# Performance work log

Hardware: AMD Instinct MI355X
Metric: run time of the kernel (lower is better)

## Reference

```python
import jax, jax.numpy as jnp
import numpy as np
from jax import lax

B, V, C, D, H, W = 1, 5, 32, 48, 128, 160
RATIO = 8


def setup_inputs() -> dict:
    key = jax.random.key(0)
    k1, k2, k3 = jax.random.split(key, 3)
    features = jax.random.normal(k1, (V, B, C, H, W), jnp.float32)
    # proj_matrices[b, v, 0] = 4x4 extrinsic, proj_matrices[b, v, 1, :3, :3] = intrinsic K
    f = 200.0
    K = np.array([[f, 0.0, W / 2.0], [0.0, f, H / 2.0], [0.0, 0.0, 1.0]], np.float32)
    proj = np.zeros((B, V, 2, 4, 4), np.float32)
    for v in range(V):
        E = np.eye(4, dtype=np.float32)
        E[0, 3] = 2.0 * v  # horizontal baseline per source view
        proj[:, v, 0] = E
        P1 = np.eye(4, dtype=np.float32)
        P1[:3, :3] = K
        proj[:, v, 1] = P1
    proj_matrices = jnp.asarray(proj)
    depth_values = jnp.broadcast_to(jnp.linspace(425.0, 935.0, D, dtype=jnp.float32), (B, D))
    mask = jax.random.normal(k2, (B, 9 * RATIO * RATIO, H, W), jnp.float32)
    W_reg = jax.random.normal(k3, (1, C, 3, 3, 3), jnp.float32) * 0.05
    return {"features": features, "proj_matrices": proj_matrices,
            "depth_values": depth_values, "mask": mask, "W_reg": W_reg}


def _combine(p):
    # p: [B,2,4,4] -> K @ E[:3,:4] written into top 3 rows of extrinsic (as in source)
    top = jnp.einsum('bij,bjk->bik', p[:, 1, :3, :3], p[:, 0, :3, :4])
    return p[:, 0].at[:, :3, :4].set(top)


def _bilinear_sample(src, x, y):
    # src [B,C,H,W]; x,y [B,P] pixel coords; zeros padding, align_corners=True
    Bs, Cs, Hs, Ws = src.shape
    x0 = jnp.floor(x)
    y0 = jnp.floor(y)
    wx = x - x0
    wy = y - y0
    src_flat = src.reshape(Bs, Cs, Hs * Ws)

    def gather(xi, yi, w):
        valid = (xi >= 0) & (xi <= Ws - 1) & (yi >= 0) & (yi <= Hs - 1)
        xi_c = jnp.clip(xi, 0, Ws - 1).astype(jnp.int32)
        yi_c = jnp.clip(yi, 0, Hs - 1).astype(jnp.int32)
        idx = (yi_c * Ws + xi_c)[:, None, :]
        vals = jnp.take_along_axis(src_flat, jnp.broadcast_to(idx, (Bs, Cs, idx.shape[-1])), axis=2)
        return vals * (w * valid)[:, None, :]

    return (gather(x0, y0, (1 - wx) * (1 - wy)) + gather(x0 + 1, y0, wx * (1 - wy))
            + gather(x0, y0 + 1, (1 - wx) * wy) + gather(x0 + 1, y0 + 1, wx * wy))


def _homo_warp(src_fea, src_proj, ref_proj, depth_values):
    # faithful homo_warping2: project ref pixel grid at each depth hypothesis into src view
    Bs, Cs, Hs, Ws = src_fea.shape
    Dd = depth_values.shape[1]
    proj = jnp.einsum('bij,bjk->bik', src_proj, jnp.linalg.inv(ref_proj))
    rot = proj[:, :3, :3]
    trans = proj[:, :3, 3]
    ys, xs = jnp.meshgrid(jnp.arange(Hs, dtype=src_fea.dtype), jnp.arange(Ws, dtype=src_fea.dtype), indexing='ij')
    xyz = jnp.stack([xs.ravel(), ys.ravel(), jnp.ones(Hs * Ws, dtype=src_fea.dtype)])  # [3,HW]
    rot_xyz = jnp.einsum('bij,jp->bip', rot, xyz)  # [B,3,HW]
    pts = rot_xyz[:, :, None, :] * depth_values[:, None, :, None] + trans[:, :, None, None]  # [B,3,D,HW]
    gx = pts[:, 0] / pts[:, 2]
    gy = pts[:, 1] / pts[:, 2]
    warped = _bilinear_sample(src_fea, gx.reshape(Bs, -1), gy.reshape(Bs, -1))
    return warped.reshape(Bs, Cs, Dd, Hs, Ws)


def _convex_upsample(depth, mask, r):
    # depth [N,1,H,W], mask [N,9*r*r,H,W] -> [N, r*H, r*W]
    N, _, Hh, Ww = depth.shape
    m = jax.nn.softmax(mask.reshape(N, 1, 9, r, r, Hh, Ww), axis=2)
    dp = jnp.pad(depth, ((0, 0), (0, 0), (1, 1), (1, 1)))
    nb = jnp.stack([dp[:, :, dy:dy + Hh, dx:dx + Ww] for dy in range(3) for dx in range(3)], axis=2)
    up = jnp.sum(m * nb[:, :, :, None, None], axis=2)  # [N,1,r,r,H,W]
    up = up.transpose(0, 1, 4, 2, 5, 3)  # [N,1,H,r,W,r]
    return up.reshape(N, r * Hh, r * Ww)


def reference(features, proj_matrices, depth_values, mask, W_reg):
    num_views = features.shape[0]
    Dd = depth_values.shape[1]
    ref_proj = _combine(proj_matrices[:, 0])
    # variance cost-volume accumulation over views (ref volume broadcast along D)
    vsum = features[0][:, :, None, :, :]
    vsq = vsum ** 2
    for v in range(1, num_views):
        src_proj = _combine(proj_matrices[:, v])
        wv = _homo_warp(features[v], src_proj, ref_proj, depth_values)
        vsum = vsum + wv
        vsq = vsq + wv * wv
    variance = vsq / num_views - (vsum / num_views) ** 2  # [B,C,D,H,W]
    # cost regularization stand-in: 3x3x3 conv C->1, SAME padding
    pre = lax.conv_general_dilated(variance, W_reg, (1, 1, 1), 'SAME',
                                   dimension_numbers=('NCDHW', 'OIDHW', 'NCDHW'))[:, 0]
    prob = jax.nn.softmax(pre, axis=1)  # [B,D,H,W]
    depth = jnp.sum(prob * depth_values[:, :, None, None], axis=1)  # [B,H,W]
    # photometric confidence (no-grad path): sliding sum of 4 along D, pad (1,2)
    pd = jnp.pad(prob, ((0, 0), (1, 2), (0, 0), (0, 0)))
    sum4 = pd[:, 0:Dd] + pd[:, 1:Dd + 1] + pd[:, 2:Dd + 2] + pd[:, 3:Dd + 3]
    di = jnp.sum(prob * jnp.arange(Dd, dtype=prob.dtype)[None, :, None, None], axis=1).astype(jnp.int32)
    di = jnp.clip(di, 0, Dd - 1)
    conf = jax.lax.stop_gradient(jnp.take_along_axis(sum4, di[:, None], axis=1)[:, 0])
    depth_up = _convex_upsample(depth[:, None], mask, RATIO)
    return (depth_up, depth, conf)
```

## Files before the change

kernel.cpp:

```cpp
#include <hip/hip_runtime.h>
#include <hip/hip_bf16.h>


#define NV 5
#define NC 32
#define ND 48
#define NH 128
#define NW 160
#define HW (NH * NW)
#define DHW (ND * HW)

typedef __attribute__((ext_vector_type(2))) float f32x2;
typedef __attribute__((ext_vector_type(4))) float f32x4;
typedef __attribute__((ext_vector_type(2), aligned(4))) float f32x2u;
typedef __attribute__((ext_vector_type(8))) unsigned short u16x8;

#define OFF_M      0
#define OFF_WF     256
#define OFF_DEPTHF 4096
#define OFF_PRE    86016
#define OFF_WV     4018176

__device__ __forceinline__ float bf2f(unsigned short u) {
  uint32_t b = ((uint32_t)u) << 16;
  float f;
  __builtin_memcpy(&f, &b, 4);
  return f;
}

__global__ void k_setup(const float* __restrict__ proj,
                        const float* __restrict__ wreg,
                        float* __restrict__ M, float* __restrict__ wf) {
  if (threadIdx.x != 0) return;
  double P[NV][2][4][4];
  for (int v = 0; v < NV; ++v)
    for (int m = 0; m < 2; ++m)
      for (int i = 0; i < 4; ++i)
        for (int j = 0; j < 4; ++j)
          P[v][m][i][j] = (double)proj[((v * 2 + m) * 4 + i) * 4 + j];
  double C[NV][4][4];
  for (int v = 0; v < NV; ++v) {
    for (int i = 0; i < 4; ++i)
      for (int j = 0; j < 4; ++j) C[v][i][j] = P[v][0][i][j];
    for (int i = 0; i < 3; ++i)
      for (int j = 0; j < 4; ++j) {
        double s = 0.0;
        for (int k = 0; k < 3; ++k) s += P[v][1][i][k] * P[v][0][k][j];
        C[v][i][j] = s;
      }
  }
  double a[4][8];
  for (int i = 0; i < 4; ++i)
    for (int j = 0; j < 4; ++j) { a[i][j] = C[0][i][j]; a[i][j + 4] = (i == j) ? 1.0 : 0.0; }
  for (int col = 0; col < 4; ++col) {
    int piv = col; double best = fabs(a[col][col]);
    for (int r = col + 1; r < 4; ++r) { double v = fabs(a[r][col]); if (v > best) { best = v; piv = r; } }
    if (piv != col)
      for (int j = 0; j < 8; ++j) { double t = a[col][j]; a[col][j] = a[piv][j]; a[piv][j] = t; }
    double pv = a[col][col];
    for (int j = 0; j < 8; ++j) a[col][j] /= pv;
    for (int r = 0; r < 4; ++r) if (r != col) {
      double f = a[r][col];
      for (int j = 0; j < 8; ++j) a[r][j] -= f * a[col][j];
    }
  }
  double inv[4][4];
  for (int i = 0; i < 4; ++i)
    for (int j = 0; j < 4; ++j) inv[i][j] = a[i][j + 4];
  for (int v = 1; v < NV; ++v) {
    float* m = M + (v - 1) * 12;
    for (int i = 0; i < 3; ++i) {
      double r[4] = {0, 0, 0, 0};
      for (int k = 0; k < 4; ++k) {
        double cv = C[v][i][k];
        for (int j = 0; j < 4; ++j) r[j] += cv * inv[k][j];
      }
      m[i * 3 + 0] = (float)r[0]; m[i * 3 + 1] = (float)r[1]; m[i * 3 + 2] = (float)r[2];
      m[9 + i] = (float)r[3];
    }
  }
  for (int c = 0; c < NC; ++c) {
    for (int t = 0; t < 27; ++t) wf[c * 28 + t] = wreg[c * 27 + t];
    wf[c * 28 + 27] = 0.f;
  }
}

__global__ __launch_bounds__(256) void k_warpvar(
    const float* __restrict__ feat,
    const float* __restrict__ depthv,
    const float* __restrict__ M,
    const float* __restrict__ wf,
    __hip_bfloat16* __restrict__ WV)
{
  int idx = blockIdx.x * 256 + threadIdx.x;
  int x = idx % NW;
  int t1 = idx / NW;
  int y = t1 % NH;
  int d = t1 / NH;
  int pix = y * NW + x;
  float xf = (float)x, yf = (float)y;
  float df = depthv[d];

  int   off[4];
  float wA[4], wB[4];
  bool any4 = false;

#pragma unroll
  for (int v = 0; v < 4; ++v) {
    const float* m = M + v * 12;
    float rx = m[0] * xf + m[1] * yf + m[2];
    float ry = m[3] * xf + m[4] * yf + m[5];
    float rz = m[6] * xf + m[7] * yf + m[8];
    float px = rx * df + m[9];
    float py = ry * df + m[10];
    float pz = rz * df + m[11];
    float gx = px / pz;
    float gy = py / pz;
    float y0 = floorf(gy);
    float wy = gy - y0;
    bool two = (wy == 0.f) || (wy == 1.f);
    any4 = any4 || !two;
    float rowf = (wy == 0.f) ? y0 : (y0 + 1.f);
    float x0 = floorf(gx);
    float wx = gx - x0;
    bool yok  = (rowf >= 0.f) && (rowf <= (float)(NH - 1));
    bool x0ok = (x0 >= 0.f) && (x0 <= (float)(NW - 1)) && yok;
    bool x1ok = (x0 >= -1.f) && (x0 <= (float)(NW - 2)) && yok;
    float rc = fminf(fmaxf(rowf, 0.f), (float)(NH - 1));
    float xc = fminf(fmaxf(x0, 0.f), (float)(NW - 1));
    int xi = (int)xc;
    int o = (int)rc * NW + xi;
    bool ddv = (o == HW - 1);
    bool sv  = (x0 >= 0.f) && (xi <= NW - 2);
    o -= ddv ? 1 : 0;
    float w0 = (1.f - wx) * (x0ok ? 1.f : 0.f);
    float w1 = wx * (x1ok ? 1.f : 0.f);
    float wsum = w0 + w1;
    wA[v] = ddv ? 0.f : (sv ? w0 : wsum);
    wB[v] = ddv ? wsum : (sv ? w1 : 0.f);
    off[v] = o;
  }

  f32x2 wv[14];
#pragma unroll
  for (int u = 0; u < 14; ++u) { wv[u].x = 0.f; wv[u].y = 0.f; }

  if (__builtin_expect(any4, 0)) {
    int cidx[16]; float cw[16];
#pragma unroll
    for (int v = 0; v < 4; ++v) {
      const float* m = M + v * 12;
      float rx = m[0] * xf + m[1] * yf + m[2];
      float ry = m[3] * xf + m[4] * yf + m[5];
      float rz = m[6] * xf + m[7] * yf + m[8];
      float px = rx * df + m[9];
      float py = ry * df + m[10];
      float pz = rz * df + m[11];
      float gx = px / pz;
      float gy = py / pz;
      float x0 = floorf(gx), y0 = floorf(gy);
      float wx = gx - x0, wy = gy - y0;
      float cxs[2] = {x0, x0 + 1.f}, cys[2] = {y0, y0 + 1.f};
      float wxs[2] = {1.f - wx, wx}, wys[2] = {1.f - wy, wy};
#pragma unroll
      for (int cy = 0; cy < 2; ++cy)
#pragma unroll
        for (int cx = 0; cx < 2; ++cx) {
          float fx = cxs[cx], fy = cys[cy];
          bool valid = (fx >= 0.f) && (fx <= (float)(NW - 1)) &&
                       (fy >= 0.f) && (fy <= (float)(NH - 1));
          float fxc = fminf(fmaxf(fx, 0.f), (float)(NW - 1));
          float fyc = fminf(fmaxf(fy, 0.f), (float)(NH - 1));
          int xi2 = (int)fxc, yi2 = (int)fyc;
          cidx[v * 4 + cy * 2 + cx] = yi2 * NW + xi2;
          cw[v * 4 + cy * 2 + cx] = wxs[cx] * wys[cy] * (valid ? 1.f : 0.f);
        }
    }
    for (int c = 0; c < NC; ++c) {
      float f0 = feat[c * HW + pix];
      float vs = f0, vq = f0 * f0;
#pragma unroll
      for (int v = 0; v < 4; ++v) {
        const float* fv = feat + ((v + 1) * NC + c) * HW;
        float val = cw[v * 4 + 0] * fv[cidx[v * 4 + 0]]
                  + cw[v * 4 + 1] * fv[cidx[v * 4 + 1]]
                  + cw[v * 4 + 2] * fv[cidx[v * 4 + 2]]
                  + cw[v * 4 + 3] * fv[cidx[v * 4 + 3]];
        vs += val;
        vq += val * val;
      }
      float var = vq * 0.2f - (vs * 0.2f) * (vs * 0.2f);
      const f32x2* wrow = (const f32x2*)(wf + c * 28);
      f32x2 vv; vv.x = var; vv.y = var;
#pragma unroll
      for (int u = 0; u < 14; ++u) wv[u] += wrow[u] * vv;
    }
  } else {
#pragma unroll
    for (int g = 0; g < NC; g += 8) {
      float f0[8];
      f32x2 e[8][4];
#pragma unroll
      for (int cc = 0; cc < 8; ++cc) {
        int c = g + cc;
        f0[cc] = feat[c * HW + pix];
#pragma unroll
        for (int v = 0; v < 4; ++v) {
          const float* fv = feat + ((v + 1) * NC + c) * HW;
          f32x2u t = *(const f32x2u*)(fv + off[v]);
          e[cc][v].x = t.x; e[cc][v].y = t.y;
        }
      }
#pragma unroll
      for (int cc = 0; cc < 8; ++cc) {
        int c = g + cc;
        float vs = f0[cc], vq = f0[cc] * f0[cc];
#pragma unroll
        for (int v = 0; v < 4; ++v) {
          float val = wA[v] * e[cc][v].x + wB[v] * e[cc][v].y;
          vs += val;
          vq += val * val;
        }
        float var = vq * 0.2f - (vs * 0.2f) * (vs * 0.2f);
        const f32x2* wrow = (const f32x2*)(wf + c * 28);
        f32x2 vv; vv.x = var; vv.y = var;
#pragma unroll
        for (int u = 0; u < 14; ++u) wv[u] += wrow[u] * vv;
      }
    }
  }

#pragma unroll
  for (int u = 0; u < 14; ++u) {
    int t0 = 2 * u;
    WV[t0 * DHW + idx] = __float2bfloat16(wv[u].x);
    if (t0 + 1 < 27) WV[(t0 + 1) * DHW + idx] = __float2bfloat16(wv[u].y);
  }
}

__global__ __launch_bounds__(256) void k_conv(const __hip_bfloat16* __restrict__ WV,
                                              float* __restrict__ pre) {
  int t8 = blockIdx.x * 256 + threadIdx.x;
  int x8 = (t8 % (NW / 8)) * 8;
  int r = t8 / (NW / 8);
  int y = r % NH;
  int d = r / NH;

  bool lo_ok = (x8 > 0);
  bool hi_ok = (x8 < NW - 8);
  int xlo = lo_ok ? x8 - 2 : 0;
  int xhi = hi_ok ? x8 + 8 : NW - 8;

  float acc[8];
#pragma unroll
  for (int k = 0; k < 8; ++k) acc[k] = 0.f;

#pragma unroll
  for (int dd = 0; dd < 3; ++dd) {
    int dp = d + dd - 1;
    bool dok = (dp >= 0) && (dp < ND);
    int dpc = min(max(dp, 0), ND - 1);
#pragma unroll
    for (int i = 0; i < 3; ++i) {
      int yp = y + i - 1;
      bool yok = (yp >= 0) && (yp < NH);
      int ypc = min(max(yp, 0), NH - 1);
      float gok = (dok && yok) ? 1.f : 0.f;
      const __hip_bfloat16* base =
          WV + (size_t)(dd * 9 + i * 3) * DHW + (size_t)dpc * HW + ypc * NW;

      u16x8 m0 = *(const u16x8*)(base + x8);
      uint32_t l0; __builtin_memcpy(&l0, base + xlo, 4);
      u16x8 m1 = *(const u16x8*)(base + DHW + x8);
      u16x8 m2 = *(const u16x8*)(base + 2 * (size_t)DHW + x8);
      uint32_t h2; __builtin_memcpy(&h2, base + 2 * (size_t)DHW + xhi, 4);

      float em1 = lo_ok ? bf2f((unsigned short)(l0 >> 16)) : 0.f;
      float e8  = hi_ok ? bf2f((unsigned short)(h2 & 0xffff)) : 0.f;

      acc[0] += gok * (em1 + bf2f(m1[0]) + bf2f(m2[1]));
#pragma unroll
      for (int k = 1; k < 7; ++k)
        acc[k] += gok * (bf2f(m0[k - 1]) + bf2f(m1[k]) + bf2f(m2[k + 1]));
      acc[7] += gok * (bf2f(m0[6]) + bf2f(m1[7]) + e8);
    }
  }

  float* op = pre + (size_t)d * HW + y * NW + x8;
  f32x4 lo4, hi4;
  lo4.x = acc[0]; lo4.y = acc[1]; lo4.z = acc[2]; lo4.w = acc[3];
  hi4.x = acc[4]; hi4.y = acc[5]; hi4.z = acc[6]; hi4.w = acc[7];
  *(f32x4*)op = lo4;
  *(f32x4*)(op + 4) = hi4;
}

__global__ __launch_bounds__(256) void k_softmax(const float* __restrict__ pre,
                                                 const float* __restrict__ depthv,
                                                 float* __restrict__ depthf,
                                                 float* __restrict__ out_depth,
                                                 float* __restrict__ out_conf) {
  int p = blockIdx.x * 256 + threadIdx.x;
  float pr[ND];
  float m = -1e30f;
#pragma unroll
  for (int d = 0; d < ND; ++d) { pr[d] = pre[d * HW + p]; m = fmaxf(m, pr[d]); }
  float s = 0.f;
#pragma unroll
  for (int d = 0; d < ND; ++d) { pr[d] = expf(pr[d] - m); s += pr[d]; }
  float inv = 1.f / s;
  float dep = 0.f, ti = 0.f;
#pragma unroll
  for (int d = 0; d < ND; ++d) {
    float prob = pr[d] * inv;
    pr[d] = prob;
    dep += prob * depthv[d];
    ti += prob * (float)d;
  }
  int di = (int)ti;
  di = di < 0 ? 0 : (di > ND - 1 ? ND - 1 : di);
  float conf = 0.f;
#pragma unroll
  for (int d = 0; d < ND; ++d)
    conf += (d >= di - 1 && d <= di + 2) ? pr[d] : 0.f;
  depthf[p] = dep;
  out_depth[p] = dep;
  out_conf[p] = conf;
}

__global__ __launch_bounds__(256) void k_upsample(const float* __restrict__ mask,
                                                  const float* __restrict__ depthf,
                                                  float* __restrict__ out) {
  int idx = blockIdx.x * 256 + threadIdx.x;
  int x = idx % NW;
  int r = idx / NW;
  int y = r % NH;
  int dy = r / NH;
  int pix = y * NW + x;

  float dv[9];
#pragma unroll
  for (int k = 0; k < 9; ++k) {
    int ky = y + k / 3 - 1;
    int kx = x + k % 3 - 1;
    bool ok = (ky >= 0) && (ky < NH) && (kx >= 0) && (kx < NW);
    int kyc = min(max(ky, 0), NH - 1);
    int kxc = min(max(kx, 0), NW - 1);
    float t = depthf[kyc * NW + kxc];
    dv[k] = ok ? t : 0.f;
  }

  float res[8];
#pragma unroll
  for (int dx = 0; dx < 8; ++dx) {
    float mv[9];
    float mmax = -1e30f;
#pragma unroll
    for (int k = 0; k < 9; ++k) {
      mv[k] = mask[(size_t)(k * 64 + dy * 8 + dx) * HW + pix];
      mmax = fmaxf(mmax, mv[k]);
    }
    float s = 0.f, acc = 0.f;
#pragma unroll
    for (int k = 0; k < 9; ++k) {
      float e = expf(mv[k] - mmax);
      s += e;
      acc += e * dv[k];
    }
    res[dx] = acc / s;
  }

  float* op = out + (size_t)(y * 8 + dy) * (NW * 8) + x * 8;
  f32x4 lo, hi;
  lo.x = res[0]; lo.y = res[1]; lo.z = res[2]; lo.w = res[3];
  hi.x = res[4]; hi.y = res[5]; hi.z = res[6]; hi.w = res[7];
  *(f32x4*)op = lo;
  *(f32x4*)(op + 4) = hi;
}

extern "C" void kernel_launch(void* const* d_in, const int* in_sizes, int n_in,
                              void* d_out, int out_size, void* d_ws, size_t ws_size,
                              hipStream_t stream) {
  const float* feat   = (const float*)d_in[0];
  const float* proj   = (const float*)d_in[1];
  const float* depthv = (const float*)d_in[2];
  const float* mask   = (const float*)d_in[3];
  const float* wreg   = (const float*)d_in[4];

  char* ws = (char*)d_ws;
  float* M       = (float*)(ws + OFF_M);
  float* wf      = (float*)(ws + OFF_WF);
  float* depthf  = (float*)(ws + OFF_DEPTHF);
  float* pre     = (float*)(ws + OFF_PRE);
  __hip_bfloat16* WV = (__hip_bfloat16*)(ws + OFF_WV);

  float* out = (float*)d_out;
  float* out_depth = out + (NH * 8) * (NW * 8);
  float* out_conf  = out_depth + HW;

  k_setup<<<1, 64, 0, stream>>>(proj, wreg, M, wf);
  k_warpvar<<<DHW / 256, 256, 0, stream>>>(feat, depthv, M, wf, WV);
  k_conv<<<(DHW / 8) / 256, 256, 0, stream>>>(WV, pre);
  k_softmax<<<HW / 256, 256, 0, stream>>>(pre, depthv, depthf, out_depth, out_conf);
  k_upsample<<<(NH * 8 * NW * 8 / 8) / 256, 256, 0, stream>>>(mask, depthf, out);
}
```

Baseline: 225.0 us.

## Compute per-tap channel contraction with bf16 MFMA instead of scalar FMAs

The variance values for each voxel (32 channels) are now packed to bf16 in LDS, and the contraction with the 27-tap conv weights is done by 16x16x32 bf16 MFMA instructions per wavefront rather than 14 vector FMAs per channel per thread. The weights are pre-laid out in bf16 MFMA B-fragment order in setup. This cuts ALU work and register pressure in the warp/variance kernel, at the cost of rounding the variance inputs to bf16 before the contraction and adding an LDS staging buffer that may lower occupancy.

```diff
diff --git a/kernel.cpp b/kernel.cpp
--- a/kernel.cpp
+++ b/kernel.cpp
@@ -14,12 +14,23 @@
 typedef __attribute__((ext_vector_type(4))) float f32x4;
 typedef __attribute__((ext_vector_type(2), aligned(4))) float f32x2u;
 typedef __attribute__((ext_vector_type(8))) unsigned short u16x8;
+typedef __attribute__((ext_vector_type(8))) short short8;
+typedef __attribute__((ext_vector_type(4))) unsigned int u32x4;
 
 #define OFF_M      0
 #define OFF_WF     256
 #define OFF_DEPTHF 4096
 #define OFF_PRE    86016
 #define OFF_WV     4018176
+#define OFF_WFB    57102336
+
+__device__ __forceinline__ uint32_t pack_bf16(float a, float b) {
+  __hip_bfloat16 ba = __float2bfloat16(a), bb = __float2bfloat16(b);
+  uint16_t ua, ub;
+  __builtin_memcpy(&ua, &ba, 2);
+  __builtin_memcpy(&ub, &bb, 2);
+  return (uint32_t)ua | ((uint32_t)ub << 16);
+}
 
 __device__ __forceinline__ float bf2f(unsigned short u) {
   uint32_t b = ((uint32_t)u) << 16;
@@ -30,7 +41,8 @@
 
 __global__ void k_setup(const float* __restrict__ proj,
                         const float* __restrict__ wreg,
-                        float* __restrict__ M, float* __restrict__ wf) {
+                        float* __restrict__ M, float* __restrict__ wf,
+                        unsigned short* __restrict__ wfB) {
   if (threadIdx.x != 0) return;
   double P[NV][2][4][4];
   for (int v = 0; v < NV; ++v)
@@ -83,16 +95,29 @@
     for (int t = 0; t < 27; ++t) wf[c * 28 + t] = wreg[c * 27 + t];
     wf[c * 28 + 27] = 0.f;
   }
+  for (int nt = 0; nt < 2; ++nt)
+    for (int l = 0; l < 64; ++l)
+      for (int e = 0; e < 8; ++e) {
+        int tap = nt * 16 + (l & 15);
+        int k = (l >> 4) * 8 + e;
+        float val = (tap < 27) ? wreg[k * 27 + tap] : 0.f;
+        __hip_bfloat16 b = __float2bfloat16(val);
+        uint16_t u; __builtin_memcpy(&u, &b, 2);
+        wfB[(nt * 64 + l) * 8 + e] = u;
+      }
 }
 
 __global__ __launch_bounds__(256) void k_warpvar(
     const float* __restrict__ feat,
     const float* __restrict__ depthv,
     const float* __restrict__ M,
-    const float* __restrict__ wf,
-    __hip_bfloat16* __restrict__ WV)
+    const unsigned short* __restrict__ wfB,
+    unsigned short* __restrict__ WVu)
 {
-  int idx = blockIdx.x * 256 + threadIdx.x;
+  __shared__ unsigned short ldsA[256 * 40];
+
+  int tid = threadIdx.x;
+  int idx = blockIdx.x * 256 + tid;
   int x = idx % NW;
   int t1 = idx / NW;
   int y = t1 % NH;
@@ -100,6 +125,10 @@
   int pix = y * NW + x;
   float xf = (float)x, yf = (float)y;
   float df = depthv[d];
+  int lane = tid & 63;
+
+  short8 bfr0 = *(const short8*)(wfB + (size_t)lane * 8);
+  short8 bfr1 = *(const short8*)(wfB + (size_t)(64 + lane) * 8);
 
   int   off[4];
   float wA[4], wB[4];
@@ -141,11 +170,42 @@
     off[v] = o;
   }
 
-  f32x2 wv[14];
-#pragma unroll
-  for (int u = 0; u < 14; ++u) { wv[u].x = 0.f; wv[u].y = 0.f; }
-
-  if (__builtin_expect(any4, 0)) {
+  if (__builtin_expect(!any4, 1)) {
+#pragma unroll
+    for (int g = 0; g < NC; g += 8) {
+      float f0[8];
+      f32x2 e[8][4];
+#pragma unroll
+      for (int cc = 0; cc < 8; ++cc) {
+        int c = g + cc;
+        f0[cc] = feat[c * HW + pix];
+#pragma unroll
+        for (int v = 0; v < 4; ++v) {
+          const float* fv = feat + ((v + 1) * NC + c) * HW;
+          f32x2u t = *(const f32x2u*)(fv + off[v]);
+          e[cc][v].x = t.x; e[cc][v].y = t.y;
+        }
+      }
+      float vr[8];
+#pragma unroll
+      for (int cc = 0; cc < 8; ++cc) {
+        float vs = f0[cc], vq = f0[cc] * f0[cc];
+#pragma unroll
+        for (int v = 0; v < 4; ++v) {
+          float val = wA[v] * e[cc][v].x + wB[v] * e[cc][v].y;
+          vs += val;
+          vq += val * val;
+        }
+        vr[cc] = vq * 0.2f - (vs * 0.2f) * (vs * 0.2f);
+      }
+      u32x4 pk;
+      pk.x = pack_bf16(vr[0], vr[1]);
+      pk.y = pack_bf16(vr[2], vr[3]);
+      pk.z = pack_bf16(vr[4], vr[5]);
+      pk.w = pack_bf16(vr[6], vr[7]);
+      *(u32x4*)(&ldsA[(size_t)tid * 40 + g]) = pk;
+    }
+  } else {
     int cidx[16]; float cw[16];
 #pragma unroll
     for (int v = 0; v < 4; ++v) {
@@ -176,65 +236,59 @@
           cw[v * 4 + cy * 2 + cx] = wxs[cx] * wys[cy] * (valid ? 1.f : 0.f);
         }
     }
-    for (int c = 0; c < NC; ++c) {
-      float f0 = feat[c * HW + pix];
-      float vs = f0, vq = f0 * f0;
-#pragma unroll
-      for (int v = 0; v < 4; ++v) {
-        const float* fv = feat + ((v + 1) * NC + c) * HW;
-        float val = cw[v * 4 + 0] * fv[cidx[v * 4 + 0]]
-                  + cw[v * 4 + 1] * fv[cidx[v * 4 + 1]]
-                  + cw[v * 4 + 2] * fv[cidx[v * 4 + 2]]
-                  + cw[v * 4 + 3] * fv[cidx[v * 4 + 3]];
-        vs += val;
-        vq += val * val;
-      }
-      float var = vq * 0.2f - (vs * 0.2f) * (vs * 0.2f);
-      const f32x2* wrow = (const f32x2*)(wf + c * 28);
-      f32x2 vv; vv.x = var; vv.y = var;
-#pragma unroll
-      for (int u = 0; u < 14; ++u) wv[u] += wrow[u] * vv;
-    }
-  } else {
-#pragma unroll
     for (int g = 0; g < NC; g += 8) {
-      float f0[8];
-      f32x2 e[8][4];
+      float vr[8];
 #pragma unroll
       for (int cc = 0; cc < 8; ++cc) {
         int c = g + cc;
-        f0[cc] = feat[c * HW + pix];
+        float f0 = feat[c * HW + pix];
+        float vs = f0, vq = f0 * f0;
 #pragma unroll
         for (int v = 0; v < 4; ++v) {
           const float* fv = feat + ((v + 1) * NC + c) * HW;
-          f32x2u t = *(const f32x2u*)(fv + off[v]);
-          e[cc][v].x = t.x; e[cc][v].y = t.y;
-        }
-      }
-#pragma unroll
-      for (int cc = 0; cc < 8; ++cc) {
-        int c = g + cc;
-        float vs = f0[cc], vq = f0[cc] * f0[cc];
-#pragma unroll
-        for (int v = 0; v < 4; ++v) {
-          float val = wA[v] * e[cc][v].x + wB[v] * e[cc][v].y;
+          float val = cw[v * 4 + 0] * fv[cidx[v * 4 + 0]]
+                    + cw[v * 4 + 1] * fv[cidx[v * 4 + 1]]
+                    + cw[v * 4 + 2] * fv[cidx[v * 4 + 2]]
+                    + cw[v * 4 + 3] * fv[cidx[v * 4 + 3]];
           vs += val;
           vq += val * val;
         }
-        float var = vq * 0.2f - (vs * 0.2f) * (vs * 0.2f);
-        const f32x2* wrow = (const f32x2*)(wf + c * 28);
-        f32x2 vv; vv.x = var; vv.y = var;
-#pragma unroll
-        for (int u = 0; u < 14; ++u) wv[u] += wrow[u] * vv;
-      }
-    }
-  }
-
-#pragma unroll
-  for (int u = 0; u < 14; ++u) {
-    int t0 = 2 * u;
-    WV[t0 * DHW + idx] = __float2bfloat16(wv[u].x);
-    if (t0 + 1 < 27) WV[(t0 + 1) * DHW + idx] = __float2bfloat16(wv[u].y);
+        vr[cc] = vq * 0.2f - (vs * 0.2f) * (vs * 0.2f);
+      }
+      u32x4 pk;
+      pk.x = pack_bf16(vr[0], vr[1]);
+      pk.y = pack_bf16(vr[2], vr[3]);
+      pk.z = pack_bf16(vr[4], vr[5]);
+      pk.w = pack_bf16(vr[6], vr[7]);
+      *(u32x4*)(&ldsA[(size_t)tid * 40 + g]) = pk;
+    }
+  }
+
+  int wb = tid & ~63;
+  int lrow = lane & 15, lk = lane >> 4;
+  uint32_t* W32 = (uint32_t*)WVu;
+  int blockbase = blockIdx.x * 256;
+
+#pragma unroll
+  for (int m = 0; m < 4; ++m) {
+    short8 af = *(const short8*)(&ldsA[(size_t)(wb + m * 16 + lrow) * 40 + lk * 8]);
+    f32x4 z = {0.f, 0.f, 0.f, 0.f};
+    f32x4 acc0 = __builtin_amdgcn_mfma_f32_16x16x32_bf16(af, bfr0, z, 0, 0, 0);
+    f32x4 acc1 = __builtin_amdgcn_mfma_f32_16x16x32_bf16(af, bfr1, z, 0, 0, 0);
+    int vox = blockbase + wb + m * 16 + lk * 4;
+    size_t o0 = ((size_t)lrow * DHW + vox) >> 1;
+    uint32_t p0 = pack_bf16(acc0[0], acc0[1]);
+    uint32_t p1 = pack_bf16(acc0[2], acc0[3]);
+    W32[o0] = p0;
+    W32[o0 + 1] = p1;
+    int tap1 = 16 + lrow;
+    if (tap1 < 27) {
+      size_t o1 = ((size_t)tap1 * DHW + vox) >> 1;
+      uint32_t q0 = pack_bf16(acc1[0], acc1[1]);
+      uint32_t q1 = pack_bf16(acc1[2], acc1[3]);
+      W32[o1] = q0;
+      W32[o1 + 1] = q1;
+    }
   }
 }
 
@@ -391,14 +445,16 @@
   float* wf      = (float*)(ws + OFF_WF);
   float* depthf  = (float*)(ws + OFF_DEPTHF);
   float* pre     = (float*)(ws + OFF_PRE);
-  __hip_bfloat16* WV = (__hip_bfloat16*)(ws + OFF_WV);
+  unsigned short* WVu = (unsigned short*)(ws + OFF_WV);
+  unsigned short* wfB = (unsigned short*)(ws + OFF_WFB);
+  const __hip_bfloat16* WV = (const __hip_bfloat16*)(ws + OFF_WV);
 
   float* out = (float*)d_out;
   float* out_depth = out + (NH * 8) * (NW * 8);
   float* out_conf  = out_depth + HW;
 
-  k_setup<<<1, 64, 0, stream>>>(proj, wreg, M, wf);
-  k_warpvar<<<DHW / 256, 256, 0, stream>>>(feat, depthv, M, wf, WV);
+  k_setup<<<1, 64, 0, stream>>>(proj, wreg, M, wf, wfB);
+  k_warpvar<<<DHW / 256, 256, 0, stream>>>(feat, depthv, M, wfB, WVu);
   k_conv<<<(DHW / 8) / 256, 256, 0, stream>>>(WV, pre);
   k_softmax<<<HW / 256, 256, 0, stream>>>(pre, depthv, depthf, out_depth, out_conf);
   k_upsample<<<(NH * 8 * NW * 8 / 8) / 256, 256, 0, stream>>>(mask, depthf, out);
```

Result: slower. 303.2 us (+34.7%).
